# Kernel tuning notes

Measured on AMD Instinct MI355X. Metric: run time of the kernel, lower is better.

The kernel has to match this reference:

```python
import jax, jax.numpy as jnp
import numpy as np

B, D, C, T, INTER = 32, 8, 64, 3000, 30
EXT = T // INTER  # extract_sequence = 100
LN_EPS = 1e-5


def _ln(x, g, b):
    # LayerNorm over last axis (channel dim c)
    mu = jnp.mean(x, axis=-1, keepdims=True)
    var = jnp.mean(jnp.square(x - mu), axis=-1, keepdims=True)
    return (x - mu) * jax.lax.rsqrt(var + LN_EPS) * g + b


def setup_inputs() -> dict:
    key = jax.random.key(0)
    ks = jax.random.split(key, 7)
    scale = 1.0 / np.sqrt(C)
    def w(k):
        return jax.random.normal(k, (C, C), jnp.float32) * scale
    def bias(k):
        return jax.random.normal(k, (C,), jnp.float32) * 0.02
    ones = jnp.ones((C,), jnp.float32)
    zeros = jnp.zeros((C,), jnp.float32)
    return {
        "x": jax.random.normal(ks[0], (B, D, C, T), jnp.float32),
        "qW": w(ks[1]), "qb": bias(ks[2]), "qg": ones, "qbeta": zeros,
        "kW": w(ks[3]), "kb": bias(ks[4]), "kg": ones, "kbeta": zeros,
        "pW": w(ks[5]), "pb": bias(ks[6]), "pg": ones, "pbeta": zeros,
    }


def reference(x, qW, qb, qg, qbeta, kW, kb, kg, kbeta, pW, pb, pg, pbeta):
    # h: [b, d, t, c]
    h = jnp.swapaxes(x, -1, -2)
    # query/key: Linear + LayerNorm over c (dropout is identity in eval)
    hq = jnp.swapaxes(_ln(h @ qW.T + qb, qg, qbeta), -1, -2)  # [b,d,c,t]
    hk = jnp.swapaxes(_ln(h @ kW.T + kb, kg, kbeta), -1, -2)  # [b,d,c,t]
    # AvgPool2d kernel=(1,INTER) stride=(1,INTER): mean over non-overlapping windows of t
    qp = hq.reshape(B, D, C, EXT, INTER).mean(-1)  # [b,d,c,e]
    kp = hk.reshape(B, D, C, EXT, INTER).mean(-1)  # [b,d,c,e]
    scaling = jnp.asarray(EXT, jnp.float32) ** 0.5
    att = jnp.einsum('bdce,bdme->bdcm', qp, kp) / scaling
    score = jax.nn.softmax(att, axis=-1)  # softmax over m
    # faithful to torch.einsum('b d c t, b d c m -> b d c t', x, score)
    out = jnp.einsum('bdct,bdcm->bdct', x, score)
    o = jnp.swapaxes(out, -1, -2)  # [b,d,t,c]
    o = _ln(o @ pW.T + pb, pg, pbeta)
    return jnp.swapaxes(o, -1, -2)  # [b,d,c,t]
```

## Files before the change

### kernel.cpp

```cpp
#include <hip/hip_runtime.h>


#define CC      64
#define TT      3000
#define TILE_T  128
#define NTB     24
#define NWG     (256 * NTB)
#define CPX     (NWG / 8)

typedef __attribute__((ext_vector_type(8)))  short short8;
typedef __attribute__((ext_vector_type(16))) float f32x16;
typedef __attribute__((ext_vector_type(4)))  float f32x4;

static __device__ __forceinline__ unsigned f2bf(float f) {
    unsigned u = __builtin_bit_cast(unsigned, f);
    return (u + 0x7FFFu + ((u >> 16) & 1u)) >> 16;
}

static __device__ __forceinline__ void load_lds16(const float* g, float* lds) {
    __builtin_amdgcn_global_load_lds(
        (const __attribute__((address_space(1))) unsigned*)g,
        (__attribute__((address_space(3))) unsigned*)lds, 16, 0, 0);
}

__global__ void pack_params(const float* __restrict__ pW,
                            const float* __restrict__ pb,
                            const float* __restrict__ pg,
                            const float* __restrict__ pbeta,
                            short* __restrict__ Wf, float* __restrict__ Pf)
{
    int i = blockIdx.x * 256 + threadIdx.x;
    if (i < 4096) {
        int e = i & 7, l = (i >> 3) & 63, f = i >> 9;
        int ct = f >> 2, kc = f & 3;
        int co = ct * 32 + (l & 31);
        int c  = kc * 16 + (l >> 5) * 8 + e;
        Wf[i] = (short)f2bf(pW[co * CC + c]);
    } else if (i < 4096 + 192) {
        int j = i - 4096;
        int a = j >> 6, q = j & 63;
        int r = q & 15, half = (q >> 4) & 1, ct = q >> 5;
        int co = ct * 32 + half * 4 + (r & 3) + 8 * (r >> 2);
        const float* src = (a == 0) ? pb : (a == 1) ? pg : pbeta;
        Pf[j] = src[co];
    }
}

__global__ __launch_bounds__(256, 4) void fused_mfma_ln(
    const float* __restrict__ x,
    const short* __restrict__ Wf,
    const float* __restrict__ Pf,
    float* __restrict__ out)
{
    __shared__ float xy[CC * TILE_T];

    const int bid = blockIdx.x;
    const int swz = (bid & 7) * CPX + (bid >> 3);
    const int bd  = swz / NTB;
    const int tb  = swz - bd * NTB;
    const int t0b = tb * TILE_T;

    const int tid  = threadIdx.x;
    const int lane = tid & 63;
    const int wid  = tid >> 6;
    const int col  = lane & 31;
    const int half = lane >> 5;

    const size_t xbase = (size_t)bd * (CC * TT);

    short8 aW[2][4];
#pragma unroll
    for (int ct = 0; ct < 2; ++ct)
#pragma unroll
        for (int kc = 0; kc < 4; ++kc)
            aW[ct][kc] = ((const short8*)Wf)[(ct * 4 + kc) * 64 + lane];

    int tq = t0b + col * 4;
    if (tq > TT - 4) tq = TT - 4;
#pragma unroll
    for (int r = 0; r < 8; ++r) {
        const int c  = r * 8 + wid * 2 + half;
        const int c0 = r * 8 + wid * 2;
        load_lds16(x + xbase + (size_t)c * TT + tq, &xy[c0 * TILE_T]);
    }
    __syncthreads();

    const int tcol = wid * 32 + col;
    short8 bx[4];
#pragma unroll
    for (int kc = 0; kc < 4; ++kc) {
        union { unsigned u[4]; short8 s; } cvt;
#pragma unroll
        for (int p = 0; p < 4; ++p) {
            const float a = xy[(kc * 16 + half * 8 + 2 * p)     * TILE_T + tcol];
            const float b = xy[(kc * 16 + half * 8 + 2 * p + 1) * TILE_T + tcol];
            cvt.u[p] = f2bf(a) | (f2bf(b) << 16);
        }
        bx[kc] = cvt.s;
    }

    f32x16 acc[2];
#pragma unroll
    for (int r = 0; r < 16; ++r) { acc[0][r] = 0.0f; acc[1][r] = 0.0f; }
#pragma unroll
    for (int kc = 0; kc < 4; ++kc) {
        acc[0] = __builtin_amdgcn_mfma_f32_32x32x16_bf16(aW[0][kc], bx[kc], acc[0], 0, 0, 0);
        acc[1] = __builtin_amdgcn_mfma_f32_32x32x16_bf16(aW[1][kc], bx[kc], acc[1], 0, 0, 0);
    }

    float s = 0.0f, s2 = 0.0f;
#pragma unroll
    for (int ct = 0; ct < 2; ++ct) {
        const float4* pbv = (const float4*)(Pf + (ct * 2 + half) * 16);
#pragma unroll
        for (int q = 0; q < 4; ++q) {
            const float4 b4 = pbv[q];
            acc[ct][q * 4 + 0] += b4.x;
            acc[ct][q * 4 + 1] += b4.y;
            acc[ct][q * 4 + 2] += b4.z;
            acc[ct][q * 4 + 3] += b4.w;
        }
#pragma unroll
        for (int r = 0; r < 16; ++r) {
            const float v = acc[ct][r];
            s += v;
            s2 = fmaf(v, v, s2);
        }
    }
    s  += __shfl_xor(s, 32);
    s2 += __shfl_xor(s2, 32);
    const float mu   = s * (1.0f / CC);
    const float rstd = rsqrtf(s2 * (1.0f / CC) - mu * mu + 1e-5f);

#pragma unroll
    for (int ct = 0; ct < 2; ++ct) {
        const float4* pgv = (const float4*)(Pf + 64  + (ct * 2 + half) * 16);
        const float4* pev = (const float4*)(Pf + 128 + (ct * 2 + half) * 16);
#pragma unroll
        for (int q = 0; q < 4; ++q) {
            const float4 g4 = pgv[q];
            const float4 e4 = pev[q];
            const float gg[4] = {g4.x, g4.y, g4.z, g4.w};
            const float ee[4] = {e4.x, e4.y, e4.z, e4.w};
#pragma unroll
            for (int j = 0; j < 4; ++j) {
                const int r  = q * 4 + j;
                const int co = ct * 32 + half * 4 + (r & 3) + 8 * (r >> 2);
                xy[co * TILE_T + tcol] = (acc[ct][r] - mu) * rstd * gg[j] + ee[j];
            }
        }
    }
    __syncthreads();

    const bool stok = (t0b + col * 4) < TT;
#pragma unroll
    for (int r = 0; r < 8; ++r) {
        const int c = r * 8 + wid * 2 + half;
        const f32x4 v = *(const f32x4*)&xy[c * TILE_T + col * 4];
        if (stok)
            __builtin_nontemporal_store(
                v, (f32x4*)(out + xbase + (size_t)c * TT + t0b + col * 4));
    }
}

extern "C" void kernel_launch(void* const* d_in, const int* in_sizes, int n_in,
                              void* d_out, int out_size, void* d_ws, size_t ws_size,
                              hipStream_t stream) {
    const float* x     = (const float*)d_in[0];
    const float* pW    = (const float*)d_in[9];
    const float* pb    = (const float*)d_in[10];
    const float* pg    = (const float*)d_in[11];
    const float* pbeta = (const float*)d_in[12];
    float* out = (float*)d_out;

    short* Wf = (short*)d_ws;
    float* Pf = (float*)((char*)d_ws + 8192);

    pack_params<<<17, 256, 0, stream>>>(pW, pb, pg, pbeta, Wf, Pf);

    dim3 grid(NWG);
    dim3 block(256);
    fused_mfma_ln<<<grid, block, 0, stream>>>(x, Wf, Pf, out);
}
```

Baseline: 68.11 us.

## Process four time tiles per workgroup with double-buffered LDS DMA pipeline

Each workgroup now handles four consecutive 128-wide time tiles instead of one, using two LDS buffers so the global-to-LDS load of the next tile overlaps compute and store of the current one. Explicit vmcnt/lgkmcnt waits and barriers sequence the stages, and the LN parameters are cached in LDS once per workgroup. This amortizes weight loads and launch overhead and hides load latency, at the cost of doubled LDS use, lower occupancy (launch bounds 2) and a fixed hand-counted wait schedule that must match the outstanding memory operations.

Result: slower. 78.38 us (+15.1%).

```diff
diff --git a/kernel.cpp b/kernel.cpp
--- a/kernel.cpp
+++ b/kernel.cpp
@@ -4,8 +4,9 @@
 #define CC      64
 #define TT      3000
 #define TILE_T  128
-#define NTB     24
-#define NWG     (256 * NTB)
+#define TPB     4
+#define BPD     6
+#define NWG     (256 * BPD)
 #define CPX     (NWG / 8)
 
 typedef __attribute__((ext_vector_type(8)))  short short8;
@@ -22,6 +23,16 @@
         (const __attribute__((address_space(1))) unsigned*)g,
         (__attribute__((address_space(3))) unsigned*)lds, 16, 0, 0);
 }
+
+#define WAIT_VM_BAR(N)                                              \
+    asm volatile("s_waitcnt vmcnt(" #N ")" ::: "memory");           \
+    __builtin_amdgcn_sched_barrier(0);                              \
+    __builtin_amdgcn_s_barrier()
+
+#define WAIT_LGKM_BAR()                                             \
+    asm volatile("s_waitcnt lgkmcnt(0)" ::: "memory");              \
+    __builtin_amdgcn_sched_barrier(0);                              \
+    __builtin_amdgcn_s_barrier()
 
 __global__ void pack_params(const float* __restrict__ pW,
                             const float* __restrict__ pb,
@@ -46,19 +57,20 @@
     }
 }
 
-__global__ __launch_bounds__(256, 4) void fused_mfma_ln(
+__global__ __launch_bounds__(256, 2) void fused_mfma_ln(
     const float* __restrict__ x,
     const short* __restrict__ Wf,
     const float* __restrict__ Pf,
     float* __restrict__ out)
 {
-    __shared__ float xy[CC * TILE_T];
-
-    const int bid = blockIdx.x;
-    const int swz = (bid & 7) * CPX + (bid >> 3);
-    const int bd  = swz / NTB;
-    const int tb  = swz - bd * NTB;
-    const int t0b = tb * TILE_T;
+    __shared__ float xy[2][CC * TILE_T];
+    __shared__ float pfl[192];
+
+    const int bid  = blockIdx.x;
+    const int swz  = (bid & 7) * CPX + (bid >> 3);
+    const int bd   = swz / BPD;
+    const int tseg = swz - bd * BPD;
+    const int t00  = tseg * (TPB * TILE_T);
 
     const int tid  = threadIdx.x;
     const int lane = tid & 63;
@@ -68,6 +80,8 @@
 
     const size_t xbase = (size_t)bd * (CC * TT);
 
+    if (tid < 192) pfl[tid] = Pf[tid];
+
     short8 aW[2][4];
 #pragma unroll
     for (int ct = 0; ct < 2; ++ct)
@@ -75,92 +89,125 @@
         for (int kc = 0; kc < 4; ++kc)
             aW[ct][kc] = ((const short8*)Wf)[(ct * 4 + kc) * 64 + lane];
 
-    int tq = t0b + col * 4;
-    if (tq > TT - 4) tq = TT - 4;
-#pragma unroll
-    for (int r = 0; r < 8; ++r) {
-        const int c  = r * 8 + wid * 2 + half;
-        const int c0 = r * 8 + wid * 2;
-        load_lds16(x + xbase + (size_t)c * TT + tq, &xy[c0 * TILE_T]);
-    }
-    __syncthreads();
-
-    const int tcol = wid * 32 + col;
-    short8 bx[4];
-#pragma unroll
-    for (int kc = 0; kc < 4; ++kc) {
-        union { unsigned u[4]; short8 s; } cvt;
-#pragma unroll
-        for (int p = 0; p < 4; ++p) {
-            const float a = xy[(kc * 16 + half * 8 + 2 * p)     * TILE_T + tcol];
-            const float b = xy[(kc * 16 + half * 8 + 2 * p + 1) * TILE_T + tcol];
-            cvt.u[p] = f2bf(a) | (f2bf(b) << 16);
-        }
-        bx[kc] = cvt.s;
-    }
-
-    f32x16 acc[2];
-#pragma unroll
-    for (int r = 0; r < 16; ++r) { acc[0][r] = 0.0f; acc[1][r] = 0.0f; }
-#pragma unroll
-    for (int kc = 0; kc < 4; ++kc) {
-        acc[0] = __builtin_amdgcn_mfma_f32_32x32x16_bf16(aW[0][kc], bx[kc], acc[0], 0, 0, 0);
-        acc[1] = __builtin_amdgcn_mfma_f32_32x32x16_bf16(aW[1][kc], bx[kc], acc[1], 0, 0, 0);
-    }
-
-    float s = 0.0f, s2 = 0.0f;
-#pragma unroll
-    for (int ct = 0; ct < 2; ++ct) {
-        const float4* pbv = (const float4*)(Pf + (ct * 2 + half) * 16);
-#pragma unroll
-        for (int q = 0; q < 4; ++q) {
-            const float4 b4 = pbv[q];
-            acc[ct][q * 4 + 0] += b4.x;
-            acc[ct][q * 4 + 1] += b4.y;
-            acc[ct][q * 4 + 2] += b4.z;
-            acc[ct][q * 4 + 3] += b4.w;
-        }
-#pragma unroll
-        for (int r = 0; r < 16; ++r) {
-            const float v = acc[ct][r];
-            s += v;
-            s2 = fmaf(v, v, s2);
-        }
-    }
-    s  += __shfl_xor(s, 32);
-    s2 += __shfl_xor(s2, 32);
-    const float mu   = s * (1.0f / CC);
-    const float rstd = rsqrtf(s2 * (1.0f / CC) - mu * mu + 1e-5f);
-
-#pragma unroll
-    for (int ct = 0; ct < 2; ++ct) {
-        const float4* pgv = (const float4*)(Pf + 64  + (ct * 2 + half) * 16);
-        const float4* pev = (const float4*)(Pf + 128 + (ct * 2 + half) * 16);
-#pragma unroll
-        for (int q = 0; q < 4; ++q) {
-            const float4 g4 = pgv[q];
-            const float4 e4 = pev[q];
-            const float gg[4] = {g4.x, g4.y, g4.z, g4.w};
-            const float ee[4] = {e4.x, e4.y, e4.z, e4.w};
-#pragma unroll
-            for (int j = 0; j < 4; ++j) {
-                const int r  = q * 4 + j;
-                const int co = ct * 32 + half * 4 + (r & 3) + 8 * (r >> 2);
-                xy[co * TILE_T + tcol] = (acc[ct][r] - mu) * rstd * gg[j] + ee[j];
-            }
-        }
-    }
-    __syncthreads();
-
-    const bool stok = (t0b + col * 4) < TT;
-#pragma unroll
-    for (int r = 0; r < 8; ++r) {
-        const int c = r * 8 + wid * 2 + half;
-        const f32x4 v = *(const f32x4*)&xy[c * TILE_T + col * 4];
-        if (stok)
-            __builtin_nontemporal_store(
-                v, (f32x4*)(out + xbase + (size_t)c * TT + t0b + col * 4));
-    }
+    auto DMASTAGE = [&](float* buf, int t0b) {
+        int tq = t0b + col * 4;
+        if (tq > TT - 4) tq = TT - 4;
+#pragma unroll
+        for (int r = 0; r < 8; ++r) {
+            const int c  = r * 8 + wid * 2 + half;
+            const int c0 = r * 8 + wid * 2;
+            load_lds16(x + xbase + (size_t)c * TT + tq, &buf[c0 * TILE_T]);
+        }
+    };
+
+    auto COMPUTE = [&](float* buf) {
+        const int tcol = wid * 32 + col;
+        short8 bx[4];
+#pragma unroll
+        for (int kc = 0; kc < 4; ++kc) {
+            union { unsigned u[4]; short8 s; } cvt;
+#pragma unroll
+            for (int p = 0; p < 4; ++p) {
+                const float a = buf[(kc * 16 + half * 8 + 2 * p)     * TILE_T + tcol];
+                const float b = buf[(kc * 16 + half * 8 + 2 * p + 1) * TILE_T + tcol];
+                cvt.u[p] = f2bf(a) | (f2bf(b) << 16);
+            }
+            bx[kc] = cvt.s;
+        }
+        f32x16 acc[2];
+#pragma unroll
+        for (int r = 0; r < 16; ++r) { acc[0][r] = 0.0f; acc[1][r] = 0.0f; }
+#pragma unroll
+        for (int kc = 0; kc < 4; ++kc) {
+            acc[0] = __builtin_amdgcn_mfma_f32_32x32x16_bf16(aW[0][kc], bx[kc], acc[0], 0, 0, 0);
+            acc[1] = __builtin_amdgcn_mfma_f32_32x32x16_bf16(aW[1][kc], bx[kc], acc[1], 0, 0, 0);
+        }
+        float s = 0.0f, s2 = 0.0f;
+#pragma unroll
+        for (int ct = 0; ct < 2; ++ct) {
+            const float4* pbv = (const float4*)(pfl + (ct * 2 + half) * 16);
+#pragma unroll
+            for (int q = 0; q < 4; ++q) {
+                const float4 b4 = pbv[q];
+                acc[ct][q * 4 + 0] += b4.x;
+                acc[ct][q * 4 + 1] += b4.y;
+                acc[ct][q * 4 + 2] += b4.z;
+                acc[ct][q * 4 + 3] += b4.w;
+            }
+#pragma unroll
+            for (int r = 0; r < 16; ++r) {
+                const float v = acc[ct][r];
+                s += v;
+                s2 = fmaf(v, v, s2);
+            }
+        }
+        s  += __shfl_xor(s, 32);
+        s2 += __shfl_xor(s2, 32);
+        const float mu   = s * (1.0f / CC);
+        const float rstd = rsqrtf(s2 * (1.0f / CC) - mu * mu + 1e-5f);
+#pragma unroll
+        for (int ct = 0; ct < 2; ++ct) {
+            const float4* pgv = (const float4*)(pfl + 64  + (ct * 2 + half) * 16);
+            const float4* pev = (const float4*)(pfl + 128 + (ct * 2 + half) * 16);
+#pragma unroll
+            for (int q = 0; q < 4; ++q) {
+                const float4 g4 = pgv[q];
+                const float4 e4 = pev[q];
+                const float gg[4] = {g4.x, g4.y, g4.z, g4.w};
+                const float ee[4] = {e4.x, e4.y, e4.z, e4.w};
+#pragma unroll
+                for (int j = 0; j < 4; ++j) {
+                    const int r  = q * 4 + j;
+                    const int co = ct * 32 + half * 4 + (r & 3) + 8 * (r >> 2);
+                    buf[co * TILE_T + tcol] = (acc[ct][r] - mu) * rstd * gg[j] + ee[j];
+                }
+            }
+        }
+    };
+
+    auto TSTORE = [&](const float* buf, int t0b) {
+        f32x4 v[8];
+#pragma unroll
+        for (int r = 0; r < 8; ++r) {
+            const int c = r * 8 + wid * 2 + half;
+            v[r] = *(const f32x4*)&buf[c * TILE_T + col * 4];
+        }
+        asm volatile("s_waitcnt lgkmcnt(0)" ::: "memory");
+        __builtin_amdgcn_sched_barrier(0);
+        const bool stok = (t0b + col * 4) < TT;
+#pragma unroll
+        for (int r = 0; r < 8; ++r) {
+            const int c = r * 8 + wid * 2 + half;
+            if (stok)
+                __builtin_nontemporal_store(
+                    v[r], (f32x4*)(out + xbase + (size_t)c * TT + t0b + col * 4));
+        }
+    };
+
+    DMASTAGE(xy[0], t00);
+    DMASTAGE(xy[1], t00 + TILE_T);
+    asm volatile("s_waitcnt vmcnt(8) lgkmcnt(0)" ::: "memory");
+    __builtin_amdgcn_sched_barrier(0);
+    __builtin_amdgcn_s_barrier();
+
+    COMPUTE(xy[0]);
+    WAIT_LGKM_BAR();
+    TSTORE(xy[0], t00);  DMASTAGE(xy[0], t00 + 2 * TILE_T);
+    WAIT_VM_BAR(16);
+
+    COMPUTE(xy[1]);
+    WAIT_LGKM_BAR();
+    TSTORE(xy[1], t00 + TILE_T);  DMASTAGE(xy[1], t00 + 3 * TILE_T);
+    WAIT_VM_BAR(16);
+
+    COMPUTE(xy[0]);
+    WAIT_LGKM_BAR();
+    TSTORE(xy[0], t00 + 2 * TILE_T);
+    WAIT_VM_BAR(8);
+
+    COMPUTE(xy[1]);
+    WAIT_LGKM_BAR();
+    TSTORE(xy[1], t00 + 3 * TILE_T);
 }
 
 extern "C" void kernel_launch(void* const* d_in, const int* in_sizes, int n_in,
```
